# Kernel tuning notes

Hardware: AMD Instinct MI355X
Metric: run time of the kernel (lower is better)

## Reference

```python
import jax, jax.numpy as jnp
from jax import lax
import numpy as np

H = 64  # hidden_size


def _gru_layer(x, w_ih, w_hh, b_ih, b_hh):
    """Single GRU layer, batch_first. x: [B, T, Din] -> [B, T, H].
    PyTorch gate order: r, z, n.
    """
    B = x.shape[0]
    # Precompute input projections for all timesteps: [B, T, 3H] -> [T, B, 3H]
    gi = jnp.einsum('bti,gi->btg', x, w_ih) + b_ih
    gi = jnp.moveaxis(gi, 1, 0)

    def step(h, g):
        gh = h @ w_hh.T + b_hh                      # [B, 3H]
        i_r, i_z, i_n = jnp.split(g, 3, axis=-1)
        h_r, h_z, h_n = jnp.split(gh, 3, axis=-1)
        r = jax.nn.sigmoid(i_r + h_r)
        z = jax.nn.sigmoid(i_z + h_z)
        n = jnp.tanh(i_n + r * h_n)
        h_new = (1.0 - z) * n + z * h
        return h_new, h_new

    h0 = jnp.zeros((B, w_hh.shape[1]), x.dtype)
    _, ys = lax.scan(step, h0, gi)                  # ys: [T, B, H]
    return jnp.moveaxis(ys, 0, 1)                   # [B, T, H]


def setup_inputs() -> dict:
    key = jax.random.key(0)
    ks = jax.random.split(key, 12)
    B, T = 4096, 512
    s = 1.0 / np.sqrt(H)  # PyTorch GRU init scale
    u = lambda k, shp: jax.random.uniform(k, shp, jnp.float32, -s, s)
    return {
        'x': jax.random.normal(ks[0], (B, T, 1), jnp.float32),
        # layer 0: input_size=1
        'w_ih0': u(ks[1], (3 * H, 1)),
        'w_hh0': u(ks[2], (3 * H, H)),
        'b_ih0': u(ks[3], (3 * H,)),
        'b_hh0': u(ks[4], (3 * H,)),
        # layer 1: input_size=H
        'w_ih1': u(ks[5], (3 * H, H)),
        'w_hh1': u(ks[6], (3 * H, H)),
        'b_ih1': u(ks[7], (3 * H,)),
        'b_hh1': u(ks[8], (3 * H,)),
        # final linear head H -> 1
        'fc_w': u(ks[9], (1, H)),
        'fc_b': u(ks[10], (1,)),
    }


def reference(x, w_ih0, w_hh0, b_ih0, b_hh0, w_ih1, w_hh1, b_ih1, b_hh1, fc_w, fc_b):
    h1 = _gru_layer(x, w_ih0, w_hh0, b_ih0, b_hh0)   # [B, T, H]
    h2 = _gru_layer(h1, w_ih1, w_hh1, b_ih1, b_hh1)  # [B, T, H]
    last = h2[:, -1, :]                              # [B, H]
    return last @ fc_w.T + fc_b                      # [B, 1]
```

## Files before the change

kernel.cpp:

```cpp
#include <hip/hip_runtime.h>


typedef _Float16 half8 __attribute__((ext_vector_type(8)));
typedef float    v4f   __attribute__((ext_vector_type(4)));
typedef float    v2f   __attribute__((ext_vector_type(2)));
typedef unsigned uint4v __attribute__((ext_vector_type(4)));

#define T_LEN 512
#define KS 72

#define L2E  1.4426950408889634f
#define L2E2 2.8853900817779268f

static __device__ __forceinline__ v4f mfma16(half8 a, half8 b, v4f c) {
    return __builtin_amdgcn_mfma_f32_16x16x32_f16(a, b, c, 0, 0, 0);
}
static __device__ __forceinline__ half8 ld8(const _Float16* p) {
    return *(const half8*)p;
}
static __device__ __forceinline__ v2f exp2v(v2f x) {
    v2f r; r.x = __builtin_amdgcn_exp2f(x.x); r.y = __builtin_amdgcn_exp2f(x.y);
    return r;
}
static __device__ __forceinline__ v2f rcpv(v2f x) {
    v2f r; r.x = __builtin_amdgcn_rcpf(x.x); r.y = __builtin_amdgcn_rcpf(x.y);
    return r;
}
static __device__ __forceinline__ v2f gru_cell2(v2f ar2, v2f az2,
                                                v2f ni2, v2f nh2, v2f h) {
    const v2f C  = exp2v(ar2);
    const v2f r  = rcpv(C + 1.0f);
    const v2f wn = __builtin_elementwise_fma(r, nh2, ni2);
    const v2f A  = exp2v(az2);
    const v2f Bv = exp2v(wn);
    const v2f aB = Bv + 1.0f;
    const v2f num = __builtin_elementwise_fma(h, aB, A * (1.0f - Bv));
    const v2f den = (A + 1.0f) * aB;
    return num * rcpv(den);
}

__global__ __launch_bounds__(512, 1)
void gru_mfma(const float* __restrict__ x,
              const float* __restrict__ w_ih0, const float* __restrict__ w_hh0,
              const float* __restrict__ b_ih0, const float* __restrict__ b_hh0,
              const float* __restrict__ w_ih1, const float* __restrict__ w_hh1,
              const float* __restrict__ b_ih1, const float* __restrict__ b_hh1,
              const float* __restrict__ fc_w,  const float* __restrict__ fc_b,
              float* __restrict__ out)
{
    __shared__ __align__(16) unsigned xh32[T_LEN * 16];
    __shared__ __align__(16) _Float16 h0f[2][16 * KS];
    __shared__ __align__(16) _Float16 h1f[2][16 * KS];
    __shared__ float red[64];

    const int tid  = threadIdx.x;
    const int wv   = tid >> 6;
    const int grp  = wv >> 2;
    const int w    = wv & 3;
    const int lane = tid & 63;
    const int n    = lane & 15;
    const int q    = lane >> 4;
    const int u    = w * 16 + n;

    const float* xg = x + (size_t)(blockIdx.x * 16) * T_LEN;
    for (int i = tid; i < 16 * T_LEN; i += 512) {
        const int row = i >> 9, t = i & 511;
        const float v = xg[row * T_LEN + t];
        xh32[t * 16 + row] =
            (unsigned)__builtin_bit_cast(unsigned short, (_Float16)v);
    }
    for (int i = tid; i < 16 * KS; i += 512) {
        h0f[1][i] = (_Float16)0;
        h1f[1][i] = (_Float16)0;
    }

    half8 B[3][4];
    {
        const int rows[3] = {u, 64 + u, 128 + u};
        const float sc[3] = {-L2E, -L2E, -L2E2};
        const float* bc[4];
        if (grp == 0) {
            bc[0] = w_hh0;      bc[1] = w_hh0 + 32;
            bc[2] = w_hh0;      bc[3] = w_hh0 + 32;
        } else {
            bc[0] = w_ih1;      bc[1] = w_ih1 + 32;
            bc[2] = w_hh1;      bc[3] = w_hh1 + 32;
        }
        #pragma unroll
        for (int g = 0; g < 3; g++)
            #pragma unroll
            for (int c = 0; c < 4; c++) {
                const float* r0 = bc[c] + rows[g] * 64 + 8 * q;
                #pragma unroll
                for (int j = 0; j < 8; j++) B[g][c][j] = (_Float16)(r0[j] * sc[g]);
            }
    }

    half8 BX[3];
    {
        const float sc3[3] = {-L2E, -L2E, -L2E2};
        #pragma unroll
        for (int g = 0; g < 3; g++) {
            uint4v z = {0u, 0u, 0u, 0u};
            if (grp == 0 && q == 0) {
                const _Float16 wv16 = (_Float16)(w_ih0[g * 64 + u] * sc3[g]);
                z.x = (unsigned)__builtin_bit_cast(unsigned short, wv16);
            }
            BX[g] = __builtin_bit_cast(half8, z);
        }
    }

    float brc, bzc, binc, bhnc;
    if (grp == 0) {
        brc = -(b_ih0[u] + b_hh0[u]) * L2E;
        bzc = -(b_ih0[64 + u] + b_hh0[64 + u]) * L2E;
        binc = -b_ih0[128 + u] * L2E2; bhnc = -b_hh0[128 + u] * L2E2;
    } else {
        brc = -(b_ih1[u] + b_hh1[u]) * L2E;
        bzc = -(b_ih1[64 + u] + b_hh1[64 + u]) * L2E;
        binc = -b_ih1[128 + u] * L2E2; bhnc = -b_hh1[128 + u] * L2E2;
    }

    const v4f biasR4  = {brc,  brc,  brc,  brc};
    const v4f biasZ4  = {bzc,  bzc,  bzc,  bzc};
    const v4f biasNi4 = {binc, binc, binc, binc};
    const v4f biasNh4 = {bhnc, bhnc, bhnc, bhnc};

    v2f hA = {0.f, 0.f}, hB = {0.f, 0.f};

    __syncthreads();

    const int abase = n * KS + 8 * q;

    #pragma unroll 1
    for (int k = 0; k < T_LEN + 1; k++) {
        if (grp == 0) {
            if (k < T_LEN) {
                const int pw = k & 1, pr = pw ^ 1;
                const half8 a0 = ld8(&h0f[pr][abase]);
                const half8 a1 = ld8(&h0f[pr][abase + 32]);
                const unsigned xw = xh32[k * 16 + n];
                uint4v ax32 = {0u, 0u, 0u, 0u};
                ax32.x = (q == 0) ? xw : 0u;
                const half8 ax = __builtin_bit_cast(half8, ax32);

                v4f accR = mfma16(ax, BX[0], biasR4);
                v4f accZ = mfma16(ax, BX[1], biasZ4);
                v4f aNi  = mfma16(ax, BX[2], biasNi4);
                v4f accN = mfma16(a0, B[2][0], biasNh4);
                accR = mfma16(a0, B[0][0], accR);
                accZ = mfma16(a0, B[1][0], accZ);
                accN = mfma16(a1, B[2][1], accN);
                accR = mfma16(a1, B[0][1], accR);
                accZ = mfma16(a1, B[1][1], accZ);

                const v2f h01 = gru_cell2((v2f){accR[0], accR[1]},
                                          (v2f){accZ[0], accZ[1]},
                                          (v2f){aNi[0],  aNi[1]},
                                          (v2f){accN[0], accN[1]}, hA);
                const v2f h23 = gru_cell2((v2f){accR[2], accR[3]},
                                          (v2f){accZ[2], accZ[3]},
                                          (v2f){aNi[2],  aNi[3]},
                                          (v2f){accN[2], accN[3]}, hB);
                hA = h01; hB = h23;
                _Float16* wp = &h0f[pw][(4 * q) * KS + u];
                wp[0]      = (_Float16)h01.x;
                wp[KS]     = (_Float16)h01.y;
                wp[2 * KS] = (_Float16)h23.x;
                wp[3 * KS] = (_Float16)h23.y;
            }
        } else {
            if (k > 0) {
                const int t = k - 1;
                const int pw = t & 1;
                const int p1 = pw ^ 1;
                const half8 g00 = ld8(&h0f[pw][abase]);
                const half8 g01 = ld8(&h0f[pw][abase + 32]);
                const half8 g10 = ld8(&h1f[p1][abase]);
                const half8 g11 = ld8(&h1f[p1][abase + 32]);

                v4f aR  = mfma16(g00, B[0][0], biasR4);
                v4f aZ  = mfma16(g00, B[1][0], biasZ4);
                v4f aNi = mfma16(g00, B[2][0], biasNi4);
                v4f aNh = mfma16(g10, B[2][2], biasNh4);
                aR  = mfma16(g01, B[0][1], aR);
                aZ  = mfma16(g01, B[1][1], aZ);
                aNi = mfma16(g01, B[2][1], aNi);
                aNh = mfma16(g11, B[2][3], aNh);
                aR  = mfma16(g10, B[0][2], aR);
                aZ  = mfma16(g10, B[1][2], aZ);
                aR  = mfma16(g11, B[0][3], aR);
                aZ  = mfma16(g11, B[1][3], aZ);

                const v2f h01 = gru_cell2((v2f){aR[0], aR[1]},
                                          (v2f){aZ[0], aZ[1]},
                                          (v2f){aNi[0], aNi[1]},
                                          (v2f){aNh[0], aNh[1]}, hA);
                const v2f h23 = gru_cell2((v2f){aR[2], aR[3]},
                                          (v2f){aZ[2], aZ[3]},
                                          (v2f){aNi[2], aNi[3]},
                                          (v2f){aNh[2], aNh[3]}, hB);
                hA = h01; hB = h23;
                _Float16* wp = &h1f[pw][(4 * q) * KS + u];
                wp[0]      = (_Float16)h01.x;
                wp[KS]     = (_Float16)h01.y;
                wp[2 * KS] = (_Float16)h23.x;
                wp[3 * KS] = (_Float16)h23.y;
            }
        }
        __syncthreads();
    }

    if (grp == 1) {
        const float fw = fc_w[u];
        const float hv[4] = {hA.x, hA.y, hB.x, hB.y};
        #pragma unroll
        for (int r = 0; r < 4; r++) {
            float v = fw * hv[r];
            v += __shfl_xor(v, 1, 64);
            v += __shfl_xor(v, 2, 64);
            v += __shfl_xor(v, 4, 64);
            v += __shfl_xor(v, 8, 64);
            if (n == 0) red[(4 * q + r) * 4 + w] = v;
        }
    }
    __syncthreads();
    if (tid < 16) {
        const float s = red[tid * 4] + red[tid * 4 + 1] + red[tid * 4 + 2] + red[tid * 4 + 3];
        out[blockIdx.x * 16 + tid] = s + fc_b[0];
    }
}

extern "C" void kernel_launch(void* const* d_in, const int* in_sizes, int n_in,
                              void* d_out, int out_size, void* d_ws, size_t ws_size,
                              hipStream_t stream)
{
    const float* x     = (const float*)d_in[0];
    const float* w_ih0 = (const float*)d_in[1];
    const float* w_hh0 = (const float*)d_in[2];
    const float* b_ih0 = (const float*)d_in[3];
    const float* b_hh0 = (const float*)d_in[4];
    const float* w_ih1 = (const float*)d_in[5];
    const float* w_hh1 = (const float*)d_in[6];
    const float* b_ih1 = (const float*)d_in[7];
    const float* b_hh1 = (const float*)d_in[8];
    const float* fc_w  = (const float*)d_in[9];
    const float* fc_b  = (const float*)d_in[10];
    float* out = (float*)d_out;

    hipLaunchKernelGGL(gru_mfma, dim3(256), dim3(512), 0, stream,
                       x, w_ih0, w_hh0, b_ih0, b_hh0,
                       w_ih1, w_hh1, b_ih1, b_hh1, fc_w, fc_b, out);
}
```

Measured before the change: 351.8 us.

## Replace per-step block barriers with LDS counter flags between layer groups

Drops the per-timestep __syncthreads that locked the two layer wave-groups together. Each wave now bumps a per-group LDS counter after writing its hidden state and spins on an acquire load of both counters. Layer-0 gets a 4-deep ring buffer so it can run up to three steps ahead of layer 1. s_setprio is also raised around the MFMA chains. The intent is to let the two layers' recurrences overlap more loosely and avoid full-block barrier stalls, at the cost of spin-wait polling and subtler memory-ordering correctness.

```diff
diff --git a/kernel.cpp b/kernel.cpp
--- a/kernel.cpp
+++ b/kernel.cpp
@@ -49,9 +49,10 @@
               float* __restrict__ out)
 {
     __shared__ __align__(16) unsigned xh32[T_LEN * 16];
-    __shared__ __align__(16) _Float16 h0f[2][16 * KS];
+    __shared__ __align__(16) _Float16 h0f[4][16 * KS];
     __shared__ __align__(16) _Float16 h1f[2][16 * KS];
     __shared__ float red[64];
+    __shared__ __align__(8) int ctr[2];
 
     const int tid  = threadIdx.x;
     const int wv   = tid >> 6;
@@ -70,9 +71,10 @@
             (unsigned)__builtin_bit_cast(unsigned short, (_Float16)v);
     }
     for (int i = tid; i < 16 * KS; i += 512) {
-        h0f[1][i] = (_Float16)0;
+        h0f[3][i] = (_Float16)0;
         h1f[1][i] = (_Float16)0;
     }
+    if (tid == 0) { ctr[0] = 0; ctr[1] = 0; }
 
     half8 B[3][4];
     {
@@ -132,84 +134,119 @@
 
     const int abase = n * KS + 8 * q;
 
+    auto wait2 = [&](int t0, int t1) __attribute__((always_inline)) {
+        for (;;) {
+            unsigned long long v = __hip_atomic_load(
+                (const unsigned long long*)ctr, __ATOMIC_ACQUIRE,
+                __HIP_MEMORY_SCOPE_WORKGROUP);
+            const int c0 = (int)(unsigned)(v & 0xffffffffull);
+            const int c1 = (int)(unsigned)(v >> 32);
+            if (c0 >= t0 && c1 >= t1) break;
+        }
+        __builtin_amdgcn_sched_barrier(0);
+    };
+    auto release = [&](int g) __attribute__((always_inline)) {
+        asm volatile("s_waitcnt lgkmcnt(0)" ::: "memory");
+        if (lane == 0)
+            __hip_atomic_fetch_add(&ctr[g], 1, __ATOMIC_RELEASE,
+                                   __HIP_MEMORY_SCOPE_WORKGROUP);
+    };
+
+    auto grp0_step = [&](int k) __attribute__((always_inline)) {
+        const _Float16* rp = &h0f[(k + 3) & 3][0];
+        _Float16*       wpbase = &h0f[k & 3][0];
+        const half8 a0 = ld8(rp + abase);
+        const half8 a1 = ld8(rp + abase + 32);
+        const unsigned xw = xh32[k * 16 + n];
+        uint4v ax32 = {0u, 0u, 0u, 0u};
+        ax32.x = (q == 0) ? xw : 0u;
+        const half8 ax = __builtin_bit_cast(half8, ax32);
+
+        __builtin_amdgcn_s_setprio(1);
+        v4f accR = mfma16(ax, BX[0], biasR4);
+        v4f accZ = mfma16(ax, BX[1], biasZ4);
+        v4f aNi  = mfma16(ax, BX[2], biasNi4);
+        v4f accN = mfma16(a0, B[2][0], biasNh4);
+        accR = mfma16(a0, B[0][0], accR);
+        accZ = mfma16(a0, B[1][0], accZ);
+        accN = mfma16(a1, B[2][1], accN);
+        accR = mfma16(a1, B[0][1], accR);
+        accZ = mfma16(a1, B[1][1], accZ);
+        __builtin_amdgcn_s_setprio(0);
+
+        const v2f h01 = gru_cell2((v2f){accR[0], accR[1]},
+                                  (v2f){accZ[0], accZ[1]},
+                                  (v2f){aNi[0],  aNi[1]},
+                                  (v2f){accN[0], accN[1]}, hA);
+        const v2f h23 = gru_cell2((v2f){accR[2], accR[3]},
+                                  (v2f){accZ[2], accZ[3]},
+                                  (v2f){aNi[2],  aNi[3]},
+                                  (v2f){accN[2], accN[3]}, hB);
+        hA = h01; hB = h23;
+        _Float16* wp = wpbase + (4 * q) * KS + u;
+        wp[0]      = (_Float16)h01.x;
+        wp[KS]     = (_Float16)h01.y;
+        wp[2 * KS] = (_Float16)h23.x;
+        wp[3 * KS] = (_Float16)h23.y;
+    };
+
+    auto grp1_step = [&](int k) __attribute__((always_inline)) {
+        const _Float16* r1 = &h1f[k & 1][0];
+        const _Float16* r0 = &h0f[(k + 3) & 3][0];
+        _Float16*       wpbase = &h1f[(k + 1) & 1][0];
+        const half8 g10 = ld8(r1 + abase);
+        const half8 g11 = ld8(r1 + abase + 32);
+        const half8 g00 = ld8(r0 + abase);
+        const half8 g01 = ld8(r0 + abase + 32);
+
+        __builtin_amdgcn_s_setprio(1);
+        v4f aR  = mfma16(g10, B[0][2], biasR4);
+        v4f aZ  = mfma16(g10, B[1][2], biasZ4);
+        v4f aNh = mfma16(g10, B[2][2], biasNh4);
+        aR  = mfma16(g11, B[0][3], aR);
+        aZ  = mfma16(g11, B[1][3], aZ);
+        aNh = mfma16(g11, B[2][3], aNh);
+        v4f aNi = mfma16(g00, B[2][0], biasNi4);
+        aR  = mfma16(g00, B[0][0], aR);
+        aZ  = mfma16(g00, B[1][0], aZ);
+        aNi = mfma16(g01, B[2][1], aNi);
+        aR  = mfma16(g01, B[0][1], aR);
+        aZ  = mfma16(g01, B[1][1], aZ);
+        __builtin_amdgcn_s_setprio(0);
+
+        const v2f h01 = gru_cell2((v2f){aR[0], aR[1]},
+                                  (v2f){aZ[0], aZ[1]},
+                                  (v2f){aNi[0], aNi[1]},
+                                  (v2f){aNh[0], aNh[1]}, hA);
+        const v2f h23 = gru_cell2((v2f){aR[2], aR[3]},
+                                  (v2f){aZ[2], aZ[3]},
+                                  (v2f){aNi[2], aNi[3]},
+                                  (v2f){aNh[2], aNh[3]}, hB);
+        hA = h01; hB = h23;
+        _Float16* wp = wpbase + (4 * q) * KS + u;
+        wp[0]      = (_Float16)h01.x;
+        wp[KS]     = (_Float16)h01.y;
+        wp[2 * KS] = (_Float16)h23.x;
+        wp[3 * KS] = (_Float16)h23.y;
+    };
+
     #pragma unroll 1
     for (int k = 0; k < T_LEN + 1; k++) {
         if (grp == 0) {
             if (k < T_LEN) {
-                const int pw = k & 1, pr = pw ^ 1;
-                const half8 a0 = ld8(&h0f[pr][abase]);
-                const half8 a1 = ld8(&h0f[pr][abase + 32]);
-                const unsigned xw = xh32[k * 16 + n];
-                uint4v ax32 = {0u, 0u, 0u, 0u};
-                ax32.x = (q == 0) ? xw : 0u;
-                const half8 ax = __builtin_bit_cast(half8, ax32);
-
-                v4f accR = mfma16(ax, BX[0], biasR4);
-                v4f accZ = mfma16(ax, BX[1], biasZ4);
-                v4f aNi  = mfma16(ax, BX[2], biasNi4);
-                v4f accN = mfma16(a0, B[2][0], biasNh4);
-                accR = mfma16(a0, B[0][0], accR);
-                accZ = mfma16(a0, B[1][0], accZ);
-                accN = mfma16(a1, B[2][1], accN);
-                accR = mfma16(a1, B[0][1], accR);
-                accZ = mfma16(a1, B[1][1], accZ);
-
-                const v2f h01 = gru_cell2((v2f){accR[0], accR[1]},
-                                          (v2f){accZ[0], accZ[1]},
-                                          (v2f){aNi[0],  aNi[1]},
-                                          (v2f){accN[0], accN[1]}, hA);
-                const v2f h23 = gru_cell2((v2f){accR[2], accR[3]},
-                                          (v2f){accZ[2], accZ[3]},
-                                          (v2f){aNi[2],  aNi[3]},
-                                          (v2f){accN[2], accN[3]}, hB);
-                hA = h01; hB = h23;
-                _Float16* wp = &h0f[pw][(4 * q) * KS + u];
-                wp[0]      = (_Float16)h01.x;
-                wp[KS]     = (_Float16)h01.y;
-                wp[2 * KS] = (_Float16)h23.x;
-                wp[3 * KS] = (_Float16)h23.y;
+                wait2(4 * k, (k >= 4) ? 4 * (k - 3) : 0);
+                grp0_step(k);
+                release(0);
             }
         } else {
             if (k > 0) {
-                const int t = k - 1;
-                const int pw = t & 1;
-                const int p1 = pw ^ 1;
-                const half8 g00 = ld8(&h0f[pw][abase]);
-                const half8 g01 = ld8(&h0f[pw][abase + 32]);
-                const half8 g10 = ld8(&h1f[p1][abase]);
-                const half8 g11 = ld8(&h1f[p1][abase + 32]);
-
-                v4f aR  = mfma16(g00, B[0][0], biasR4);
-                v4f aZ  = mfma16(g00, B[1][0], biasZ4);
-                v4f aNi = mfma16(g00, B[2][0], biasNi4);
-                v4f aNh = mfma16(g10, B[2][2], biasNh4);
-                aR  = mfma16(g01, B[0][1], aR);
-                aZ  = mfma16(g01, B[1][1], aZ);
-                aNi = mfma16(g01, B[2][1], aNi);
-                aNh = mfma16(g11, B[2][3], aNh);
-                aR  = mfma16(g10, B[0][2], aR);
-                aZ  = mfma16(g10, B[1][2], aZ);
-                aR  = mfma16(g11, B[0][3], aR);
-                aZ  = mfma16(g11, B[1][3], aZ);
-
-                const v2f h01 = gru_cell2((v2f){aR[0], aR[1]},
-                                          (v2f){aZ[0], aZ[1]},
-                                          (v2f){aNi[0], aNi[1]},
-                                          (v2f){aNh[0], aNh[1]}, hA);
-                const v2f h23 = gru_cell2((v2f){aR[2], aR[3]},
-                                          (v2f){aZ[2], aZ[3]},
-                                          (v2f){aNi[2], aNi[3]},
-                                          (v2f){aNh[2], aNh[3]}, hB);
-                hA = h01; hB = h23;
-                _Float16* wp = &h1f[pw][(4 * q) * KS + u];
-                wp[0]      = (_Float16)h01.x;
-                wp[KS]     = (_Float16)h01.y;
-                wp[2 * KS] = (_Float16)h23.x;
-                wp[3 * KS] = (_Float16)h23.y;
-            }
-        }
-        __syncthreads();
-    }
+                wait2(4 * k, 4 * (k - 1));
+                grp1_step(k);
+                release(1);
+            }
+        }
+    }
+    __syncthreads();
 
     if (grp == 1) {
         const float fw = fc_w[u];
```

Measured after the change: 334.5 us. 1.05x faster.
